# Optimization experiments

Hardware: AMD Instinct MI355X
Metric: run time of the kernel (lower is better)

## Reference

```python
import jax, jax.numpy as jnp
import numpy as np

B, S, D, H = 4, 2048, 1024, 16
HD = D // H

def setup_inputs() -> dict:
    key = jax.random.key(0)
    ks = jax.random.split(key, 5)
    scale = 1.0 / np.sqrt(D)
    x = jax.random.normal(ks[0], (B, S, D), dtype=jnp.float32)
    w_qkv = jax.random.normal(ks[1], (D, 3 * D), dtype=jnp.float32) * scale
    b_qkv = jax.random.normal(ks[2], (3 * D,), dtype=jnp.float32) * 0.01
    w_proj = jax.random.normal(ks[3], (D, D), dtype=jnp.float32) * scale
    b_proj = jax.random.normal(ks[4], (D,), dtype=jnp.float32) * 0.01
    return {"x": x, "w_qkv": w_qkv, "b_qkv": b_qkv, "w_proj": w_proj, "b_proj": b_proj}

def reference(x, w_qkv, b_qkv, w_proj, b_proj):
    b, s, d = x.shape
    qkv = x @ w_qkv + b_qkv                      # [B,S,3D]
    qkv = qkv.reshape(b, s, 3, H, HD)
    q, k, v = jnp.moveaxis(qkv, 2, 0)            # each [B,S,H,HD]
    q = q.transpose(0, 2, 1, 3)                  # [B,H,S,HD]
    k = k.transpose(0, 2, 1, 3)
    v = v.transpose(0, 2, 1, 3)
    scale = 1.0 / jnp.sqrt(jnp.asarray(HD, dtype=x.dtype))
    scores = jnp.einsum('bhqd,bhkd->bhqk', q, k) * scale
    attn = jax.nn.softmax(scores, axis=-1)
    out = jnp.einsum('bhqk,bhkd->bhqd', attn, v)  # [B,H,S,HD]
    out = out.transpose(0, 2, 1, 3).reshape(b, s, d)
    return out @ w_proj + b_proj
```

## Files before the change

kernel.cpp:

```cpp
#include <hip/hip_runtime.h>

#define B_  4
#define S_  2048
#define D_  1024
#define H_  16
#define HD_ 64
#define M_  (B_*S_)
#define QSCALE 0.1803368801111204f

typedef unsigned short u16;
typedef __bf16 bf16x8 __attribute__((ext_vector_type(8)));
typedef __bf16 bf16x2 __attribute__((ext_vector_type(2)));
typedef float  f32x4  __attribute__((ext_vector_type(4)));
typedef float  f32x16 __attribute__((ext_vector_type(16)));

__device__ __forceinline__ u16 f2bf(float f) {
  unsigned int u = __float_as_uint(f);
  u += 0x7fffu + ((u >> 16) & 1u);
  return (u16)(u >> 16);
}
__device__ __forceinline__ unsigned int packbf2(float lo, float hi) {
#if __has_builtin(__builtin_amdgcn_cvt_pk_bf16_f32)
  union { bf16x2 v; unsigned int u; } c;
  c.v = __builtin_amdgcn_cvt_pk_bf16_f32(lo, hi);
  return c.u;
#else
  return (unsigned int)f2bf(lo) | ((unsigned int)f2bf(hi) << 16);
#endif
}
__device__ __forceinline__ void gld16(const void* g, void* l) {
  __builtin_amdgcn_global_load_lds(
      (const __attribute__((address_space(1))) unsigned int*)g,
      (__attribute__((address_space(3))) unsigned int*)l, 16, 0, 0);
}
#define WAIT_VM6() asm volatile("s_waitcnt vmcnt(6)" ::: "memory")
#define WAIT_VM0() asm volatile("s_waitcnt vmcnt(0)" ::: "memory")
#define LGKM0()    asm volatile("s_waitcnt lgkmcnt(0)" ::: "memory")
#define MFMA32(a,b,c) __builtin_amdgcn_mfma_f32_32x32x16_bf16(a,b,c,0,0,0)
#define MFMA16(a,b,c) __builtin_amdgcn_mfma_f32_16x16x32_bf16(a,b,c,0,0,0)

__device__ __forceinline__ size_t off16e(int r, int k) {
  return ((size_t)((r >> 7) * 32 + (k >> 5))) * 4096
       + (size_t)((r >> 4) & 7) * 512
       + (size_t)(((k >> 3) & 3) * 16 + (r & 15)) * 8 + (k & 7);
}
__device__ __forceinline__ size_t offA32(int bh, int s, int hd) {
  return ((size_t)(bh * 32 + (s >> 6)) * 8 + ((s >> 5) & 1) * 4 + (hd >> 4)) * 512
       + (size_t)(((hd >> 3) & 1) * 32 + (s & 31)) * 8 + (hd & 7);
}
__device__ __forceinline__ size_t offVT(int bh, int s, int hd) {
  return ((size_t)(bh * 32 + (s >> 6)) * 8 + (hd >> 5) * 4 + ((s >> 4) & 3)) * 512
       + (size_t)(((s >> 3) & 1) * 32 + (hd & 31)) * 8 + (s & 7);
}

__global__ void cvt_f32_bf16(const float* __restrict__ in, u16* __restrict__ out, int n4) {
  int i = blockIdx.x * 256 + threadIdx.x;
  if (i < n4) {
    float4 v = ((const float4*)in)[i];
    int m = i >> 8;
    int k = (i & 255) * 4;
    *(uint2*)&out[off16e(m, k)] = make_uint2(packbf2(v.x, v.y), packbf2(v.z, v.w));
  }
}

__global__ void transpose_w(const float* __restrict__ in, u16* __restrict__ out, int R, int C) {
  __shared__ float tile[32][33];
  int c0 = blockIdx.x * 32, r0 = blockIdx.y * 32;
  int tx = threadIdx.x, ty = threadIdx.y;
  #pragma unroll
  for (int i = 0; i < 4; i++)
    tile[ty + i*8][tx] = in[(size_t)(r0 + ty + i*8) * C + c0 + tx];
  __syncthreads();
  #pragma unroll
  for (int i = 0; i < 4; i++)
    out[off16e(c0 + ty + i*8, r0 + tx)] = f2bf(tile[tx][ty + i*8]);
}

#define STAGE_A(h, tau, dbuf) \
  { const u16* s_ = Asrc[h] + (size_t)(2*(tau))*4096 + t*8; \
    char* d_ = (char*)(As + (((dbuf)*2 + (h))*2)*4096) + w*1024; \
    gld16(s_, d_); gld16(s_ + 4096, d_ + 8192); }
#define STAGE_B(h, tau, dbuf) \
  { const u16* s_ = Bsrc[h] + (size_t)(2*(tau))*4096 + t*8; \
    char* d_ = (char*)(Bs + (((dbuf)*2 + (h))*2)*4096) + w*1024; \
    gld16(s_, d_); gld16(s_ + 4096, d_ + 8192); }

__device__ __forceinline__ void gemm_mainloop256(
    const u16* const Asrc[2], const u16* const Bsrc[2],
    u16* As, u16* Bs, f32x4 (&acc)[2][2][4][2],
    const int t, const int w, const int l)
{
  const int frA = (w >> 2) * 4;
  const int frB = (w & 3) * 2;

  STAGE_A(0, 0, 0); STAGE_B(0, 0, 0); STAGE_B(1, 0, 0); STAGE_A(1, 0, 0);
  STAGE_A(0, 1, 1); STAGE_B(0, 1, 1); STAGE_B(1, 1, 1);
  WAIT_VM6();
  __builtin_amdgcn_s_barrier();

  bf16x8 aR[2][4], b0R[2][2], b1R[2][2];
  for (int kt = 0; kt < 16; ++kt) {
    const int bu = kt & 1, nb = bu ^ 1;
    const u16* Abuf = As + (bu*2)*2*4096;
    const u16* Bbuf = Bs + (bu*2)*2*4096;

    #pragma unroll
    for (int kk = 0; kk < 2; ++kk) {
      #pragma unroll
      for (int mt = 0; mt < 4; ++mt)
        aR[kk][mt] = *(const bf16x8*)(Abuf + (0*2 + kk)*4096 + (frA + mt)*512 + l*8);
      #pragma unroll
      for (int nt = 0; nt < 2; ++nt)
        b0R[kk][nt] = *(const bf16x8*)(Bbuf + (0*2 + kk)*4096 + (frB + nt)*512 + l*8);
    }
    if (kt < 15) STAGE_A(1, kt+1, nb);
    __builtin_amdgcn_s_barrier();
    LGKM0();
    __builtin_amdgcn_s_setprio(1);
    #pragma unroll
    for (int mt = 0; mt < 4; ++mt)
      #pragma unroll
      for (int nt = 0; nt < 2; ++nt)
        #pragma unroll
        for (int kk = 0; kk < 2; ++kk)
          acc[0][0][mt][nt] = MFMA16(aR[kk][mt], b0R[kk][nt], acc[0][0][mt][nt]);
    __builtin_amdgcn_s_setprio(0);
    __builtin_amdgcn_s_barrier();

    #pragma unroll
    for (int kk = 0; kk < 2; ++kk)
      #pragma unroll
      for (int nt = 0; nt < 2; ++nt)
        b1R[kk][nt] = *(const bf16x8*)(Bbuf + (1*2 + kk)*4096 + (frB + nt)*512 + l*8);
    if (kt < 14) STAGE_A(0, kt+2, bu);
    __builtin_amdgcn_s_barrier();
    LGKM0();
    __builtin_amdgcn_s_setprio(1);
    #pragma unroll
    for (int mt = 0; mt < 4; ++mt)
      #pragma unroll
      for (int nt = 0; nt < 2; ++nt)
        #pragma unroll
        for (int kk = 0; kk < 2; ++kk)
          acc[0][1][mt][nt] = MFMA16(aR[kk][mt], b1R[kk][nt], acc[0][1][mt][nt]);
    __builtin_amdgcn_s_setprio(0);
    __builtin_amdgcn_s_barrier();

    #pragma unroll
    for (int kk = 0; kk < 2; ++kk)
      #pragma unroll
      for (int mt = 0; mt < 4; ++mt)
        aR[kk][mt] = *(const bf16x8*)(Abuf + (1*2 + kk)*4096 + (frA + mt)*512 + l*8);
    if (kt < 14) STAGE_B(0, kt+2, bu);
    __builtin_amdgcn_s_barrier();
    LGKM0();
    __builtin_amdgcn_s_setprio(1);
    #pragma unroll
    for (int mt = 0; mt < 4; ++mt)
      #pragma unroll
      for (int nt = 0; nt < 2; ++nt)
        #pragma unroll
        for (int kk = 0; kk < 2; ++kk)
          acc[1][0][mt][nt] = MFMA16(aR[kk][mt], b0R[kk][nt], acc[1][0][mt][nt]);
    __builtin_amdgcn_s_setprio(0);
    __builtin_amdgcn_s_barrier();

    if (kt < 14) STAGE_B(1, kt+2, bu);
    __builtin_amdgcn_s_barrier();
    __builtin_amdgcn_s_setprio(1);
    #pragma unroll
    for (int mt = 0; mt < 4; ++mt)
      #pragma unroll
      for (int nt = 0; nt < 2; ++nt)
        #pragma unroll
        for (int kk = 0; kk < 2; ++kk)
          acc[1][1][mt][nt] = MFMA16(aR[kk][mt], b1R[kk][nt], acc[1][1][mt][nt]);
    __builtin_amdgcn_s_setprio(0);
    if (kt <= 13)      { WAIT_VM6(); }
    else if (kt == 14) { WAIT_VM0(); }
    __builtin_amdgcn_s_barrier();
  }
}

__global__ __launch_bounds__(512,2) void gemm_qkv(
    const u16* __restrict__ X, const u16* __restrict__ WT,
    const float* __restrict__ bias,
    u16* __restrict__ qb, u16* __restrict__ kb, u16* __restrict__ vb)
{
  __shared__ u16 As[2*2*2*4096];
  __shared__ u16 Bs[2*2*2*4096];
  const int t = threadIdx.x, w = t >> 6, l = t & 63;
  const int i = blockIdx.x, xcd = i & 7, j = i >> 3;
  const int byi = xcd * 4 + (j & 3);
  const int bxi = j >> 2;
  const int m0 = byi * 256, n0 = bxi * 256;
  const u16* Asrc[2] = { X  + (size_t)(2*byi + 0)*32*4096,
                         X  + (size_t)(2*byi + 1)*32*4096 };
  const u16* Bsrc[2] = { WT + (size_t)(2*bxi + 0)*32*4096,
                         WT + (size_t)(2*bxi + 1)*32*4096 };

  f32x4 acc[2][2][4][2] = {};
  gemm_mainloop256(Asrc, Bsrc, As, Bs, acc, t, w, l);

  const int lr = l & 15, quad = l >> 4;
  const int wr = (w >> 2) * 64, wc = (w & 3) * 32;
  #pragma unroll
  for (int MH = 0; MH < 2; MH++)
  #pragma unroll
  for (int NH = 0; NH < 2; NH++)
  #pragma unroll
  for (int mt = 0; mt < 4; mt++)
  #pragma unroll
  for (int nt = 0; nt < 2; nt++) {
    int n = n0 + NH*128 + wc + nt*16 + lr;
    float bia = bias[n];
    int which = n >> 10, hh = (n >> 6) & 15, hd = n & 63;
    #pragma unroll
    for (int r = 0; r < 4; r++) {
      int m = m0 + MH*128 + wr + mt*16 + quad*4 + r;
      float v = acc[MH][NH][mt][nt][r] + bia;
      int bb = m >> 11, s = m & 2047, bh = bb * 16 + hh;
      if (which == 0)      qb[offA32(bh, s, hd)] = f2bf(v * QSCALE);
      else if (which == 1) kb[offA32(bh, s, hd)] = f2bf(v);
      else                 vb[offVT(bh, s, hd)] = f2bf(v);
    }
  }
}

__global__ __launch_bounds__(512,2) void gemm_proj(
    const u16* __restrict__ X, const u16* __restrict__ WT,
    const float* __restrict__ bias, float* __restrict__ out)
{
  __shared__ u16 As[2*2*2*4096];
  __shared__ u16 Bs[2*2*2*4096];
  const int t = threadIdx.x, w = t >> 6, l = t & 63;
  const int i = blockIdx.x, xcd = i & 7, j = i >> 3;
  const int byi = xcd * 4 + (j & 3);
  const int bxi = j >> 2;
  const int m0 = byi * 256, n0 = bxi * 256;
  const u16* Asrc[2] = { X  + (size_t)(2*byi + 0)*32*4096,
                         X  + (size_t)(2*byi + 1)*32*4096 };
  const u16* Bsrc[2] = { WT + (size_t)(2*bxi + 0)*32*4096,
                         WT + (size_t)(2*bxi + 1)*32*4096 };

  f32x4 acc[2][2][4][2] = {};
  gemm_mainloop256(Asrc, Bsrc, As, Bs, acc, t, w, l);

  const int lr = l & 15, quad = l >> 4;
  const int wr = (w >> 2) * 64, wc = (w & 3) * 32;
  #pragma unroll
  for (int MH = 0; MH < 2; MH++)
  #pragma unroll
  for (int NH = 0; NH < 2; NH++)
  #pragma unroll
  for (int mt = 0; mt < 4; mt++)
  #pragma unroll
  for (int nt = 0; nt < 2; nt++) {
    int n = n0 + NH*128 + wc + nt*16 + lr;
    float bia = bias[n];
    #pragma unroll
    for (int r = 0; r < 4; r++) {
      int m = m0 + MH*128 + wr + mt*16 + quad*4 + r;
      out[(size_t)m * D_ + n] = acc[MH][NH][mt][nt][r] + bia;
    }
  }
}

__global__ __launch_bounds__(256,4) void attn(
    const u16* __restrict__ qb, const u16* __restrict__ kb,
    const u16* __restrict__ vt, u16* __restrict__ ob)
{
  __shared__ u16 Ks[2][8*512];
  __shared__ u16 Vs[2][8*512];
  const int t = threadIdx.x, w = t >> 6, l = t & 63, l31 = l & 31, h = l >> 5;
  const int i = blockIdx.x, xcd = i & 7, j = i >> 3;
  const int bh = xcd * 8 + (j >> 4), qt = j & 15;
  const int b = bh >> 4, hh = bh & 15;
  const int s0 = qt * 128 + w * 32;
  const u16* qp = qb + (size_t)bh * 131072;
  const u16* kp = kb + (size_t)bh * 131072;
  const u16* vp = vt + (size_t)bh * 131072;

  bf16x8 qa[4];
  {
    const size_t qbase = ((size_t)(qt*2 + (w >> 1)) * 8 + (w & 1) * 4) * 512;
    #pragma unroll
    for (int kk = 0; kk < 4; kk++)
      qa[kk] = *(const bf16x8*)(qp + qbase + (size_t)kk * 512 + l*8);
  }

  union { unsigned int u[4]; bf16x8 v; } ones;
  ones.u[0] = ones.u[1] = ones.u[2] = ones.u[3] = 0x3F803F80u;

  f32x16 o[2] = {};
  f32x16 lacc = {};

  #pragma unroll
  for (int c = 0; c < 2; c++) {
    gld16(kp + (size_t)(w*2 + c) * 512 + l*8, (char*)&Ks[0][0] + (w*2 + c)*1024);
    gld16(vp + (size_t)(w*2 + c) * 512 + l*8, (char*)&Vs[0][0] + (w*2 + c)*1024);
  }
  WAIT_VM0();
  __syncthreads();

  for (int kt = 0; kt < 32; kt++) {
    const int cur = kt & 1, nxt = cur ^ 1;
    const u16* Kb = &Ks[cur][0];
    const u16* Vb = &Vs[cur][0];

    if (kt < 31) {
      const size_t gs = (size_t)(kt + 1) * 4096;
      #pragma unroll
      for (int c = 0; c < 2; c++) {
        gld16(kp + gs + (size_t)(w*2 + c) * 512 + l*8, (char*)&Ks[nxt][0] + (w*2 + c)*1024);
        gld16(vp + gs + (size_t)(w*2 + c) * 512 + l*8, (char*)&Vs[nxt][0] + (w*2 + c)*1024);
      }
    }

    f32x16 sf[2] = {};
    #pragma unroll
    for (int kk = 0; kk < 4; kk++) {
      bf16x8 ka0 = *(const bf16x8*)(Kb + (0*4 + kk)*512 + l*8);
      bf16x8 ka1 = *(const bf16x8*)(Kb + (1*4 + kk)*512 + l*8);
      sf[0] = MFMA32(ka0, qa[kk], sf[0]);
      sf[1] = MFMA32(ka1, qa[kk], sf[1]);
    }

    unsigned int pk[2][4][2];
    #pragma unroll
    for (int mt = 0; mt < 2; mt++)
      #pragma unroll
      for (int e = 0; e < 4; e++) {
        float p0 = __builtin_amdgcn_exp2f(sf[mt][4*e+0]);
        float p1 = __builtin_amdgcn_exp2f(sf[mt][4*e+1]);
        float p2 = __builtin_amdgcn_exp2f(sf[mt][4*e+2]);
        float p3 = __builtin_amdgcn_exp2f(sf[mt][4*e+3]);
        pk[mt][e][0] = packbf2(p0, p1);
        pk[mt][e][1] = packbf2(p2, p3);
      }

    #pragma unroll
    for (int kk2 = 0; kk2 < 4; kk2++) {
      const int mt = kk2 >> 1, k1 = kk2 & 1;
      bf16x8 bv0 = *(const bf16x8*)(Vb + (0*4 + kk2)*512 + l*8);
      bf16x8 bv1 = *(const bf16x8*)(Vb + (1*4 + kk2)*512 + l*8);
      union { unsigned int u[4]; bf16x8 v; } pa;
#if __has_builtin(__builtin_amdgcn_permlane32_swap)
      auto s02 = __builtin_amdgcn_permlane32_swap(pk[mt][2*k1][0], pk[mt][2*k1+1][0], false, false);
      auto s13 = __builtin_amdgcn_permlane32_swap(pk[mt][2*k1][1], pk[mt][2*k1+1][1], false, false);
      pa.u[0] = s02[0]; pa.u[1] = s13[0]; pa.u[2] = s02[1]; pa.u[3] = s13[1];
#else
      unsigned int s0_ = h ? pk[mt][2*k1][0] : pk[mt][2*k1+1][0];
      unsigned int s1_ = h ? pk[mt][2*k1][1] : pk[mt][2*k1+1][1];
      unsigned int r0 = (unsigned int)__shfl_xor((int)s0_, 32);
      unsigned int r1 = (unsigned int)__shfl_xor((int)s1_, 32);
      pa.u[0] = h ? r0 : pk[mt][2*k1][0];
      pa.u[1] = h ? r1 : pk[mt][2*k1][1];
      pa.u[2] = h ? pk[mt][2*k1+1][0] : r0;
      pa.u[3] = h ? pk[mt][2*k1+1][1] : r1;
#endif
      o[0] = MFMA32(pa.v, bv0, o[0]);
      o[1] = MFMA32(pa.v, bv1, o[1]);
      lacc = MFMA32(pa.v, ones.v, lacc);
    }

    if (kt < 31) {
      WAIT_VM0();
      __syncthreads();
    }
  }

  #pragma unroll
  for (int rb = 0; rb < 4; rb++) {
    #pragma unroll
    for (int c = 0; c < 4; c++) {
      int r = rb*4 + c;
      float iv = 1.f / lacc[r];
      int row = s0 + c + 8*rb + 4*h;
      int m = b * S_ + row;
      int d0 = hh*64 + l31, d1 = hh*64 + 32 + l31;
      ob[off16e(m, d0)] = f2bf(o[0][r] * iv);
      ob[off16e(m, d1)] = f2bf(o[1][r] * iv);
    }
  }
}

extern "C" void kernel_launch(void* const* d_in, const int* in_sizes, int n_in,
                              void* d_out, int out_size, void* d_ws, size_t ws_size,
                              hipStream_t stream) {
  const float* x      = (const float*)d_in[0];
  const float* w_qkv  = (const float*)d_in[1];
  const float* b_qkv  = (const float*)d_in[2];
  const float* w_proj = (const float*)d_in[3];
  const float* b_proj = (const float*)d_in[4];
  float* out = (float*)d_out;

  char* ws = (char*)d_ws;
  u16* xbf    = (u16*)ws; ws += (size_t)M_ * D_ * 2;
  u16* wqkvT  = (u16*)ws; ws += (size_t)3 * D_ * D_ * 2;
  u16* wprojT = (u16*)ws; ws += (size_t)D_ * D_ * 2;
  u16* qbuf   = (u16*)ws; ws += (size_t)M_ * D_ * 2;
  u16* kbuf   = (u16*)ws; ws += (size_t)M_ * D_ * 2;
  u16* vtbuf  = (u16*)ws; ws += (size_t)M_ * D_ * 2;
  u16* aobuf  = (u16*)ws; ws += (size_t)M_ * D_ * 2;

  cvt_f32_bf16<<<(M_ * D_ / 4 + 255) / 256, 256, 0, stream>>>(x, xbf, M_ * D_ / 4);
  transpose_w<<<dim3(3 * D_ / 32, D_ / 32), dim3(32, 8), 0, stream>>>(w_qkv, wqkvT, D_, 3 * D_);
  transpose_w<<<dim3(D_ / 32, D_ / 32), dim3(32, 8), 0, stream>>>(w_proj, wprojT, D_, D_);
  gemm_qkv<<<384, 512, 0, stream>>>(xbf, wqkvT, b_qkv, qbuf, kbuf, vtbuf);
  attn<<<1024, 256, 0, stream>>>(qbuf, kbuf, vtbuf, aobuf);
  gemm_proj<<<128, 512, 0, stream>>>(aobuf, wprojT, b_proj, out);
}
```

Before: 307.9 us.

## Merge prep kernels into one launch and retile output projection to 128x128

```diff
diff --git a/kernel.cpp b/kernel.cpp
--- a/kernel.cpp
+++ b/kernel.cpp
@@ -34,6 +34,7 @@
       (__attribute__((address_space(3))) unsigned int*)l, 16, 0, 0);
 }
 #define WAIT_VM6() asm volatile("s_waitcnt vmcnt(6)" ::: "memory")
+#define WAIT_VM4() asm volatile("s_waitcnt vmcnt(4)" ::: "memory")
 #define WAIT_VM0() asm volatile("s_waitcnt vmcnt(0)" ::: "memory")
 #define LGKM0()    asm volatile("s_waitcnt lgkmcnt(0)" ::: "memory")
 #define MFMA32(a,b,c) __builtin_amdgcn_mfma_f32_32x32x16_bf16(a,b,c,0,0,0)
@@ -53,20 +54,12 @@
        + (size_t)(((s >> 3) & 1) * 32 + (hd & 31)) * 8 + (s & 7);
 }
 
-__global__ void cvt_f32_bf16(const float* __restrict__ in, u16* __restrict__ out, int n4) {
-  int i = blockIdx.x * 256 + threadIdx.x;
-  if (i < n4) {
-    float4 v = ((const float4*)in)[i];
-    int m = i >> 8;
-    int k = (i & 255) * 4;
-    *(uint2*)&out[off16e(m, k)] = make_uint2(packbf2(v.x, v.y), packbf2(v.z, v.w));
-  }
-}
-
-__global__ void transpose_w(const float* __restrict__ in, u16* __restrict__ out, int R, int C) {
+__device__ __forceinline__ void transpose_body(
+    const float* __restrict__ in, u16* __restrict__ out,
+    int C, int bx, int by, int tx, int ty)
+{
   __shared__ float tile[32][33];
-  int c0 = blockIdx.x * 32, r0 = blockIdx.y * 32;
-  int tx = threadIdx.x, ty = threadIdx.y;
+  int c0 = bx * 32, r0 = by * 32;
   #pragma unroll
   for (int i = 0; i < 4; i++)
     tile[ty + i*8][tx] = in[(size_t)(r0 + ty + i*8) * C + c0 + tx];
@@ -74,6 +67,26 @@
   #pragma unroll
   for (int i = 0; i < 4; i++)
     out[off16e(c0 + ty + i*8, r0 + tx)] = f2bf(tile[tx][ty + i*8]);
+}
+
+__global__ void prep(const float* __restrict__ x, u16* __restrict__ xbf,
+                     const float* __restrict__ w_qkv, u16* __restrict__ wqkvT,
+                     const float* __restrict__ w_proj, u16* __restrict__ wprojT)
+{
+  const int tx = threadIdx.x, ty = threadIdx.y, bid = blockIdx.x;
+  if (bid < 8192) {
+    int i = bid * 256 + ty * 32 + tx;
+    float4 v = ((const float4*)x)[i];
+    int m = i >> 8;
+    int k = (i & 255) * 4;
+    *(uint2*)&xbf[off16e(m, k)] = make_uint2(packbf2(v.x, v.y), packbf2(v.z, v.w));
+  } else if (bid < 8192 + 3072) {
+    int idx = bid - 8192;
+    transpose_body(w_qkv, wqkvT, 3 * D_, idx % 96, idx / 96, tx, ty);
+  } else {
+    int idx = bid - 8192 - 3072;
+    transpose_body(w_proj, wprojT, D_, idx % 32, idx / 32, tx, ty);
+  }
 }
 
 #define STAGE_A(h, tau, dbuf) \
@@ -227,41 +240,95 @@
   }
 }
 
-__global__ __launch_bounds__(512,2) void gemm_proj(
+__device__ __forceinline__ void gemm_mainloop128(
+    const u16* __restrict__ Ab, const u16* __restrict__ Bb,
+    u16* As, u16* Bs,
+    f32x4 (&acc)[4][4], const int t, const int w, const int l)
+{
+  const int wm4 = (w >> 1) * 4;
+  const int wn4 = (w & 1) * 4;
+
+  #pragma unroll
+  for (int kg = 0; kg < 2; ++kg) {
+    const size_t gs = (size_t)kg * 4096;
+    gld16(Ab + gs + t*8,        (char*)(As + kg*4096) + w*1024);
+    gld16(Ab + gs + 2048 + t*8, (char*)(As + kg*4096) + 4096 + w*1024);
+    gld16(Bb + gs + t*8,        (char*)(Bs + kg*4096) + w*1024);
+    gld16(Bb + gs + 2048 + t*8, (char*)(Bs + kg*4096) + 4096 + w*1024);
+  }
+  WAIT_VM0();
+  __syncthreads();
+
+  for (int kt = 0; kt < 16; ++kt) {
+    const int cur = kt & 1, nxt = cur ^ 1;
+    #pragma unroll
+    for (int kk = 0; kk < 2; ++kk) {
+      bf16x8 a[4], b[4];
+      const u16* Ar = As + (cur*2 + kk)*4096;
+      const u16* Br = Bs + (cur*2 + kk)*4096;
+      #pragma unroll
+      for (int mt = 0; mt < 4; ++mt)
+        a[mt] = *(const bf16x8*)(Ar + (wm4 + mt)*512 + l*8);
+      #pragma unroll
+      for (int nt = 0; nt < 4; ++nt)
+        b[nt] = *(const bf16x8*)(Br + (wn4 + nt)*512 + l*8);
+
+      if (kt < 15) {
+        const size_t gs = (size_t)((kt + 1)*2 + kk) * 4096;
+        u16* Ad = As + (nxt*2 + kk)*4096;
+        u16* Bd = Bs + (nxt*2 + kk)*4096;
+        gld16(Ab + gs + t*8,        (char*)Ad + w*1024);
+        gld16(Ab + gs + 2048 + t*8, (char*)Ad + 4096 + w*1024);
+        gld16(Bb + gs + t*8,        (char*)Bd + w*1024);
+        gld16(Bb + gs + 2048 + t*8, (char*)Bd + 4096 + w*1024);
+      }
+
+      __builtin_amdgcn_s_barrier();
+      LGKM0();
+      __builtin_amdgcn_s_setprio(1);
+      #pragma unroll
+      for (int mt = 0; mt < 4; ++mt)
+        #pragma unroll
+        for (int nt = 0; nt < 4; ++nt)
+          acc[mt][nt] = MFMA16(a[mt], b[nt], acc[mt][nt]);
+      __builtin_amdgcn_s_setprio(0);
+
+      if (kt < 15)      { WAIT_VM4(); }
+      else if (kk == 0) { WAIT_VM0(); }
+      __builtin_amdgcn_s_barrier();
+    }
+  }
+}
+
+__global__ __launch_bounds__(256,2) void gemm_proj(
     const u16* __restrict__ X, const u16* __restrict__ WT,
     const float* __restrict__ bias, float* __restrict__ out)
 {
-  __shared__ u16 As[2*2*2*4096];
-  __shared__ u16 Bs[2*2*2*4096];
+  __shared__ u16 As[2*2*4096];
+  __shared__ u16 Bs[2*2*4096];
   const int t = threadIdx.x, w = t >> 6, l = t & 63;
-  const int i = blockIdx.x, xcd = i & 7, j = i >> 3;
-  const int byi = xcd * 4 + (j & 3);
-  const int bxi = j >> 2;
-  const int m0 = byi * 256, n0 = bxi * 256;
-  const u16* Asrc[2] = { X  + (size_t)(2*byi + 0)*32*4096,
-                         X  + (size_t)(2*byi + 1)*32*4096 };
-  const u16* Bsrc[2] = { WT + (size_t)(2*bxi + 0)*32*4096,
-                         WT + (size_t)(2*bxi + 1)*32*4096 };
-
-  f32x4 acc[2][2][4][2] = {};
-  gemm_mainloop256(Asrc, Bsrc, As, Bs, acc, t, w, l);
-
-  const int lr = l & 15, quad = l >> 4;
-  const int wr = (w >> 2) * 64, wc = (w & 3) * 32;
-  #pragma unroll
-  for (int MH = 0; MH < 2; MH++)
-  #pragma unroll
-  for (int NH = 0; NH < 2; NH++)
+  const int orig = blockIdx.x;
+  const int xcd = orig & 7, j = orig >> 3;
+  const int bxi = j >> 3;
+  const int byi = xcd * 8 + (j & 7);
+  const int m0 = byi * 128, n0 = bxi * 128;
+  const u16* Ab = X  + (size_t)byi * 32 * 4096;
+  const u16* Bb = WT + (size_t)bxi * 32 * 4096;
+
+  f32x4 acc[4][4] = {};
+  gemm_mainloop128(Ab, Bb, As, Bs, acc, t, w, l);
+
+  const int wm = (w >> 1) * 64, wn = (w & 1) * 64, lr = l & 15, quad = l >> 4;
   #pragma unroll
   for (int mt = 0; mt < 4; mt++)
   #pragma unroll
-  for (int nt = 0; nt < 2; nt++) {
-    int n = n0 + NH*128 + wc + nt*16 + lr;
+  for (int nt = 0; nt < 4; nt++) {
+    int n = n0 + wn + nt * 16 + lr;
     float bia = bias[n];
     #pragma unroll
     for (int r = 0; r < 4; r++) {
-      int m = m0 + MH*128 + wr + mt*16 + quad*4 + r;
-      out[(size_t)m * D_ + n] = acc[MH][NH][mt][nt][r] + bia;
+      int m = m0 + wm + mt * 16 + quad * 4 + r;
+      out[(size_t)m * D_ + n] = acc[mt][nt][r] + bia;
     }
   }
 }
@@ -404,10 +471,8 @@
   u16* vtbuf  = (u16*)ws; ws += (size_t)M_ * D_ * 2;
   u16* aobuf  = (u16*)ws; ws += (size_t)M_ * D_ * 2;
 
-  cvt_f32_bf16<<<(M_ * D_ / 4 + 255) / 256, 256, 0, stream>>>(x, xbf, M_ * D_ / 4);
-  transpose_w<<<dim3(3 * D_ / 32, D_ / 32), dim3(32, 8), 0, stream>>>(w_qkv, wqkvT, D_, 3 * D_);
-  transpose_w<<<dim3(D_ / 32, D_ / 32), dim3(32, 8), 0, stream>>>(w_proj, wprojT, D_, D_);
+  prep<<<8192 + 3072 + 1024, dim3(32, 8), 0, stream>>>(x, xbf, w_qkv, wqkvT, w_proj, wprojT);
   gemm_qkv<<<384, 512, 0, stream>>>(xbf, wqkvT, b_qkv, qbuf, kbuf, vtbuf);
   attn<<<1024, 256, 0, stream>>>(qbuf, kbuf, vtbuf, aobuf);
-  gemm_proj<<<128, 512, 0, stream>>>(aobuf, wprojT, b_proj, out);
-}
+  gemm_proj<<<512, 256, 0, stream>>>(aobuf, wprojT, b_proj, out);
+}
```

After: 290.9 us. -5.5%, faster.
